# Optimization experiments

Measured on AMD Instinct MI355X. Metric: run time of the kernel, lower is better.

The kernel has to match this reference:

```python
import jax, jax.numpy as jnp
import numpy as np

B, C, D = 512, 1000, 512
K = 10


def setup_inputs() -> dict:
    key = jax.random.key(0)
    k1, k2, k3, k4, k5 = jax.random.split(key, 5)
    x = jax.random.normal(k1, (B, D), dtype=jnp.float32)
    protos = jax.random.normal(k2, (C, D), dtype=jnp.float32)
    # ex2/ex1 chosen so N*ex2^2 - ex1^2 > 0 (valid sqrt)
    ex2 = jax.random.uniform(k3, (C, D), dtype=jnp.float32) + 1.0
    ex1 = jax.random.uniform(k4, (C, D), dtype=jnp.float32) * 0.1
    cls_num = jax.random.randint(k5, (C,), 1, 100, dtype=jnp.int32)
    proto_label = jnp.arange(C, dtype=jnp.int32)
    return {"x": x, "protos": protos, "ex2": ex2, "ex1": ex1,
            "cls_num": cls_num, "proto_label": proto_label, "k_nearest": K}


def reference(x, protos, ex2, ex1, cls_num, proto_label, k_nearest):
    # rd: per-class, per-feature variance proxy  [C, D]
    N = cls_num[:, None].astype(ex2.dtype)
    rd = jnp.sqrt(N * ex2 ** 2 - ex1 ** 2)
    # softmax over feature dim of (rowmax - rd)
    rd = jax.nn.softmax(jnp.max(rd, axis=1, keepdims=True) - rd, axis=1)
    # weighted squared distances: [B, C, D] -> reduce D -> [B, C]
    diff = x[:, None, :] - protos[None, :, :]
    x_dists = diff ** 2 * rd[None, :, :]
    simi_mat = x_dists.sum(axis=2)  # [B, C]
    # k smallest distances (torch.topk largest=False)
    neg_vals, topk_index = jax.lax.top_k(-simi_mat, k_nearest)
    topk_vals = -neg_vals  # [B, K]
    topk_conf = topk_vals.sum(axis=1, keepdims=True) / topk_vals  # [B, K]
    # pick prototype with max confidence, map through label table
    temp = jnp.argmax(topk_conf, axis=1)  # [B]
    ans_index = jnp.take_along_axis(topk_index, temp[:, None], axis=1)[:, 0]
    predict = proto_label[ans_index]  # [B]
    return predict, topk_conf
```

## Files before the change

kernel.cpp:

```cpp
#include <hip/hip_runtime.h>
#include <math.h>
#include <float.h>

#define B_SZ 512
#define C_SZ 1000
#define D_SZ 512
#define K_TOP 10
#define K2 1024

#define SIMI_OFF 0

#define BM 128
#define BN 16
#define BK 64
#define LDB 1032

using f16x8 = __attribute__((ext_vector_type(8))) _Float16;
using f32x4 = __attribute__((ext_vector_type(4))) float;

#if __has_builtin(__builtin_amdgcn_exp2f)
#define FAST_EXP2(x) __builtin_amdgcn_exp2f(x)
#else
#define FAST_EXP2(x) exp2f(x)
#endif
#if __has_builtin(__builtin_amdgcn_sqrtf)
#define FAST_SQRT(x) __builtin_amdgcn_sqrtf(x)
#else
#define FAST_SQRT(x) sqrtf(x)
#endif
#define LOG2E 1.44269504088896340736f

__device__ __forceinline__ void split2(float v, _Float16& h, _Float16& l) {
    h = (_Float16)v;
    l = (_Float16)(v - (float)h);
}

__global__ __launch_bounds__(512, 4) void fused_kernel(const float* __restrict__ x,
                                                       const float* __restrict__ protos,
                                                       const float* __restrict__ ex2,
                                                       const float* __restrict__ ex1,
                                                       const int* __restrict__ cls_num,
                                                       float* __restrict__ simi) {
    __shared__ __align__(16) _Float16 BSh[BN][LDB];
    __shared__ __align__(16) _Float16 BSl[BN][LDB];
    __shared__ float t3s[BN];

    const int tid  = threadIdx.x;
    const int lane = tid & 63;
    const int w    = tid >> 6;
    const int cx = blockIdx.x & 63;
    const int by = blockIdx.x >> 6;
    const int c0 = cx * BN;
    const int b0 = by * BM;
    if (c0 >= C_SZ) return;

    const int mw = w * 16;
    const int lr = lane & 15;
    const int kg = lane >> 4;

    const float* xrow = x + (size_t)(b0 + mw + lr) * D_SZ;

    auto load_a = [&](int ch, float4* d) {
        const int kx = (ch < 8 ? ch * BK : ch * BK - D_SZ) + kg * 8;
        const float* xp = xrow + kx;
        d[0] = *(const float4*)(xp);
        d[1] = *(const float4*)(xp + 4);
        d[2] = *(const float4*)(xp + 32);
        d[3] = *(const float4*)(xp + 36);
    };

    float4 cur[4], nxt[4];
    load_a(0, cur);

    #pragma unroll
    for (int r = 0; r < 2; r++) {
        const int lc = w * 2 + r;
        const int c  = c0 + lc;
        if (c < C_SZ) {
            const size_t rb = (size_t)c * D_SZ + lane * 8;
            float e2v[8], e1v[8], pv[8];
            *(float4*)&e2v[0] = *(const float4*)(ex2 + rb);
            *(float4*)&e2v[4] = *(const float4*)(ex2 + rb + 4);
            *(float4*)&e1v[0] = *(const float4*)(ex1 + rb);
            *(float4*)&e1v[4] = *(const float4*)(ex1 + rb + 4);
            *(float4*)&pv[0]  = *(const float4*)(protos + rb);
            *(float4*)&pv[4]  = *(const float4*)(protos + rb + 4);
            const float N = (float)cls_num[c];

            float v[8], mn = FLT_MAX;
            #pragma unroll
            for (int k = 0; k < 8; k++) {
                v[k] = FAST_SQRT(N * e2v[k] * e2v[k] - e1v[k] * e1v[k]);
                mn = fminf(mn, v[k]);
            }
            #pragma unroll
            for (int off = 1; off < 64; off <<= 1) mn = fminf(mn, __shfl_xor(mn, off));

            float ev[8], s = 0.f, te = 0.f;
            #pragma unroll
            for (int k = 0; k < 8; k++) {
                ev[k] = FAST_EXP2((mn - v[k]) * LOG2E);
                s += ev[k];
                te = fmaf(ev[k] * pv[k], pv[k], te);
            }
            #pragma unroll
            for (int off = 1; off < 64; off <<= 1) {
                s  += __shfl_xor(s, off);
                te += __shfl_xor(te, off);
            }
            const float inv = 1.0f / s;
            if (lane == 0) t3s[lc] = te * inv;

            f16x8 h1, l1, h2, l2;
            #pragma unroll
            for (int k = 0; k < 8; k++) {
                const float rdv = ev[k] * inv;
                const float w2  = -2.0f * rdv * pv[k];
                _Float16 hh, ll;
                split2(rdv, hh, ll); h1[k] = hh; l1[k] = ll;
                split2(w2,  hh, ll); h2[k] = hh; l2[k] = ll;
            }
            const int d = lane * 8;
            *(f16x8*)&BSh[lc][d]         = h1;
            *(f16x8*)&BSh[lc][D_SZ + d]  = h2;
            *(f16x8*)&BSl[lc][d]         = l1;
            *(f16x8*)&BSl[lc][D_SZ + d]  = l2;
        } else {
            f16x8 z;
            #pragma unroll
            for (int k = 0; k < 8; k++) z[k] = (_Float16)0.f;
            const int d = lane * 8;
            *(f16x8*)&BSh[lc][d]        = z;
            *(f16x8*)&BSh[lc][D_SZ + d] = z;
            *(f16x8*)&BSl[lc][d]        = z;
            *(f16x8*)&BSl[lc][D_SZ + d] = z;
        }
    }
    __syncthreads();

    f32x4 acc;
    #pragma unroll
    for (int r = 0; r < 4; r++) acc[r] = 0.f;

    for (int ch = 0; ch < K2 / BK; ch++) {
        if (ch + 1 < K2 / BK) load_a(ch + 1, nxt);

        float av[16];
        *(float4*)&av[0]  = cur[0];
        *(float4*)&av[4]  = cur[1];
        *(float4*)&av[8]  = cur[2];
        *(float4*)&av[12] = cur[3];
        if (ch < 8) {
            #pragma unroll
            for (int k = 0; k < 16; k++) av[k] *= av[k];
        }
        f16x8 ah0, al0, ah1, al1;
        #pragma unroll
        for (int k = 0; k < 8; k++) {
            _Float16 hh, ll;
            split2(av[k], hh, ll);     ah0[k] = hh; al0[k] = ll;
            split2(av[k + 8], hh, ll); ah1[k] = hh; al1[k] = ll;
        }

        const int kb = ch * BK + kg * 8;
        {
            const f16x8 fbh = *(const f16x8*)&BSh[lr][kb];
            const f16x8 fbl = *(const f16x8*)&BSl[lr][kb];
            acc = __builtin_amdgcn_mfma_f32_16x16x32_f16(al0, fbl, acc, 0, 0, 0);
            acc = __builtin_amdgcn_mfma_f32_16x16x32_f16(ah0, fbl, acc, 0, 0, 0);
            acc = __builtin_amdgcn_mfma_f32_16x16x32_f16(al0, fbh, acc, 0, 0, 0);
            acc = __builtin_amdgcn_mfma_f32_16x16x32_f16(ah0, fbh, acc, 0, 0, 0);
        }
        {
            const f16x8 fbh = *(const f16x8*)&BSh[lr][kb + 32];
            const f16x8 fbl = *(const f16x8*)&BSl[lr][kb + 32];
            acc = __builtin_amdgcn_mfma_f32_16x16x32_f16(al1, fbl, acc, 0, 0, 0);
            acc = __builtin_amdgcn_mfma_f32_16x16x32_f16(ah1, fbl, acc, 0, 0, 0);
            acc = __builtin_amdgcn_mfma_f32_16x16x32_f16(al1, fbh, acc, 0, 0, 0);
            acc = __builtin_amdgcn_mfma_f32_16x16x32_f16(ah1, fbh, acc, 0, 0, 0);
        }

        if (ch + 1 < K2 / BK) {
            cur[0] = nxt[0]; cur[1] = nxt[1];
            cur[2] = nxt[2]; cur[3] = nxt[3];
        }
    }

    const int c = c0 + lr;
    if (c < C_SZ) {
        const float t3v = t3s[lr];
        #pragma unroll
        for (int r = 0; r < 4; r++) {
            const int b = b0 + mw + kg * 4 + r;
            simi[(size_t)b * C_SZ + c] = acc[r] + t3v;
        }
    }
}

__global__ __launch_bounds__(256) void topk_kernel(const float* __restrict__ ws,
                                                   const int* __restrict__ proto_label,
                                                   float* __restrict__ out) {
    const float* simi = ws + SIMI_OFF;
    const int wid = threadIdx.x >> 6;
    const int lane = threadIdx.x & 63;
    const int b = blockIdx.x * 4 + wid;

    float vals[16];
    #pragma unroll
    for (int j = 0; j < 16; j++) {
        const int c = lane + j * 64;
        vals[j] = (c < C_SZ) ? simi[(size_t)b * C_SZ + c] : FLT_MAX;
    }

    float kv[K_TOP];
    int ki[K_TOP];
    for (int t = 0; t < K_TOP; t++) {
        float bv = FLT_MAX;
        int bi = 0x7fffffff;
        #pragma unroll
        for (int j = 0; j < 16; j++) {
            const int c = lane + j * 64;
            if (vals[j] < bv) { bv = vals[j]; bi = c; }
        }
        #pragma unroll
        for (int off = 1; off < 64; off <<= 1) {
            const float ov = __shfl_xor(bv, off);
            const int oi = __shfl_xor(bi, off);
            if (ov < bv || (ov == bv && oi < bi)) { bv = ov; bi = oi; }
        }
        kv[t] = bv;
        ki[t] = bi;
        if ((bi & 63) == lane) vals[bi >> 6] = FLT_MAX;
    }

    if (lane == 0) {
        float S = 0.f;
        #pragma unroll
        for (int t = 0; t < K_TOP; t++) S += kv[t];
        float conf[K_TOP];
        #pragma unroll
        for (int t = 0; t < K_TOP; t++) {
            conf[t] = S / kv[t];
            out[B_SZ + b * K_TOP + t] = conf[t];
        }
        int best = 0;
        for (int t = 1; t < K_TOP; t++)
            if (conf[t] > conf[best]) best = t;
        out[b] = (float)proto_label[ki[best]];
    }
}

extern "C" void kernel_launch(void* const* d_in, const int* in_sizes, int n_in,
                              void* d_out, int out_size, void* d_ws, size_t ws_size,
                              hipStream_t stream) {
    const float* x           = (const float*)d_in[0];
    const float* protos      = (const float*)d_in[1];
    const float* ex2         = (const float*)d_in[2];
    const float* ex1         = (const float*)d_in[3];
    const int*   cls_num     = (const int*)d_in[4];
    const int*   proto_label = (const int*)d_in[5];

    float* ws  = (float*)d_ws;
    float* out = (float*)d_out;

    fused_kernel<<<256, 512, 0, stream>>>(x, protos, ex2, ex1, cls_num,
                                          ws + SIMI_OFF);

    topk_kernel<<<B_SZ / 4, 256, 0, stream>>>(ws, proto_label, out);
}
```

Measured before the change: 96.35 us.

## Halve class tile to 8 per block and load x once per chunk

The fused distance kernel now handles 8 classes per block instead of 16. The MFMA B tile is padded with zero rows, and the grid is a 2D 125x4 launch with no out-of-range blocks, so 500 blocks run instead of 256 and work is spread over more CUs. The main loop now loads each x chunk once and feeds both x^2 and x into the MFMAs, halving the global reads of x per block. The cost is that half of each 16-wide MFMA computes padding, and the per-block prototype preprocessing is repeated across more blocks.

```diff
diff --git a/kernel.cpp b/kernel.cpp
--- a/kernel.cpp
+++ b/kernel.cpp
@@ -11,8 +11,8 @@
 #define SIMI_OFF 0
 
 #define BM 128
-#define BN 16
-#define BK 64
+#define BN 8
+#define BNP 16
 #define LDB 1032
 
 using f16x8 = __attribute__((ext_vector_type(8))) _Float16;
@@ -41,18 +41,17 @@
                                                        const float* __restrict__ ex1,
                                                        const int* __restrict__ cls_num,
                                                        float* __restrict__ simi) {
-    __shared__ __align__(16) _Float16 BSh[BN][LDB];
-    __shared__ __align__(16) _Float16 BSl[BN][LDB];
+    __shared__ __align__(16) _Float16 BSh[BNP][LDB];
+    __shared__ __align__(16) _Float16 BSl[BNP][LDB];
     __shared__ float t3s[BN];
 
     const int tid  = threadIdx.x;
     const int lane = tid & 63;
     const int w    = tid >> 6;
-    const int cx = blockIdx.x & 63;
-    const int by = blockIdx.x >> 6;
+    const int cx = blockIdx.x;
+    const int by = blockIdx.y;
     const int c0 = cx * BN;
     const int b0 = by * BM;
-    if (c0 >= C_SZ) return;
 
     const int mw = w * 16;
     const int lr = lane & 15;
@@ -61,8 +60,7 @@
     const float* xrow = x + (size_t)(b0 + mw + lr) * D_SZ;
 
     auto load_a = [&](int ch, float4* d) {
-        const int kx = (ch < 8 ? ch * BK : ch * BK - D_SZ) + kg * 8;
-        const float* xp = xrow + kx;
+        const float* xp = xrow + ch * 64 + kg * 8;
         d[0] = *(const float4*)(xp);
         d[1] = *(const float4*)(xp + 4);
         d[2] = *(const float4*)(xp + 32);
@@ -72,69 +70,65 @@
     float4 cur[4], nxt[4];
     load_a(0, cur);
 
-    #pragma unroll
-    for (int r = 0; r < 2; r++) {
-        const int lc = w * 2 + r;
+    {
+        const int lc = w;
         const int c  = c0 + lc;
-        if (c < C_SZ) {
-            const size_t rb = (size_t)c * D_SZ + lane * 8;
-            float e2v[8], e1v[8], pv[8];
-            *(float4*)&e2v[0] = *(const float4*)(ex2 + rb);
-            *(float4*)&e2v[4] = *(const float4*)(ex2 + rb + 4);
-            *(float4*)&e1v[0] = *(const float4*)(ex1 + rb);
-            *(float4*)&e1v[4] = *(const float4*)(ex1 + rb + 4);
-            *(float4*)&pv[0]  = *(const float4*)(protos + rb);
-            *(float4*)&pv[4]  = *(const float4*)(protos + rb + 4);
-            const float N = (float)cls_num[c];
-
-            float v[8], mn = FLT_MAX;
-            #pragma unroll
-            for (int k = 0; k < 8; k++) {
-                v[k] = FAST_SQRT(N * e2v[k] * e2v[k] - e1v[k] * e1v[k]);
-                mn = fminf(mn, v[k]);
-            }
-            #pragma unroll
-            for (int off = 1; off < 64; off <<= 1) mn = fminf(mn, __shfl_xor(mn, off));
-
-            float ev[8], s = 0.f, te = 0.f;
-            #pragma unroll
-            for (int k = 0; k < 8; k++) {
-                ev[k] = FAST_EXP2((mn - v[k]) * LOG2E);
-                s += ev[k];
-                te = fmaf(ev[k] * pv[k], pv[k], te);
-            }
-            #pragma unroll
-            for (int off = 1; off < 64; off <<= 1) {
-                s  += __shfl_xor(s, off);
-                te += __shfl_xor(te, off);
-            }
-            const float inv = 1.0f / s;
-            if (lane == 0) t3s[lc] = te * inv;
-
-            f16x8 h1, l1, h2, l2;
-            #pragma unroll
-            for (int k = 0; k < 8; k++) {
-                const float rdv = ev[k] * inv;
-                const float w2  = -2.0f * rdv * pv[k];
-                _Float16 hh, ll;
-                split2(rdv, hh, ll); h1[k] = hh; l1[k] = ll;
-                split2(w2,  hh, ll); h2[k] = hh; l2[k] = ll;
-            }
-            const int d = lane * 8;
-            *(f16x8*)&BSh[lc][d]         = h1;
-            *(f16x8*)&BSh[lc][D_SZ + d]  = h2;
-            *(f16x8*)&BSl[lc][d]         = l1;
-            *(f16x8*)&BSl[lc][D_SZ + d]  = l2;
-        } else {
-            f16x8 z;
-            #pragma unroll
-            for (int k = 0; k < 8; k++) z[k] = (_Float16)0.f;
-            const int d = lane * 8;
-            *(f16x8*)&BSh[lc][d]        = z;
-            *(f16x8*)&BSh[lc][D_SZ + d] = z;
-            *(f16x8*)&BSl[lc][d]        = z;
-            *(f16x8*)&BSl[lc][D_SZ + d] = z;
-        }
+        const size_t rb = (size_t)c * D_SZ + lane * 8;
+        float e2v[8], e1v[8], pv[8];
+        *(float4*)&e2v[0] = *(const float4*)(ex2 + rb);
+        *(float4*)&e2v[4] = *(const float4*)(ex2 + rb + 4);
+        *(float4*)&e1v[0] = *(const float4*)(ex1 + rb);
+        *(float4*)&e1v[4] = *(const float4*)(ex1 + rb + 4);
+        *(float4*)&pv[0]  = *(const float4*)(protos + rb);
+        *(float4*)&pv[4]  = *(const float4*)(protos + rb + 4);
+        const float N = (float)cls_num[c];
+
+        float v[8], mn = FLT_MAX;
+        #pragma unroll
+        for (int k = 0; k < 8; k++) {
+            v[k] = FAST_SQRT(N * e2v[k] * e2v[k] - e1v[k] * e1v[k]);
+            mn = fminf(mn, v[k]);
+        }
+        #pragma unroll
+        for (int off = 1; off < 64; off <<= 1) mn = fminf(mn, __shfl_xor(mn, off));
+
+        float ev[8], s = 0.f, te = 0.f;
+        #pragma unroll
+        for (int k = 0; k < 8; k++) {
+            ev[k] = FAST_EXP2((mn - v[k]) * LOG2E);
+            s += ev[k];
+            te = fmaf(ev[k] * pv[k], pv[k], te);
+        }
+        #pragma unroll
+        for (int off = 1; off < 64; off <<= 1) {
+            s  += __shfl_xor(s, off);
+            te += __shfl_xor(te, off);
+        }
+        const float inv = 1.0f / s;
+        if (lane == 0) t3s[lc] = te * inv;
+
+        f16x8 h1, l1, h2, l2;
+        #pragma unroll
+        for (int k = 0; k < 8; k++) {
+            const float rdv = ev[k] * inv;
+            const float w2  = -2.0f * rdv * pv[k];
+            _Float16 hh, ll;
+            split2(rdv, hh, ll); h1[k] = hh; l1[k] = ll;
+            split2(w2,  hh, ll); h2[k] = hh; l2[k] = ll;
+        }
+        const int d = lane * 8;
+        *(f16x8*)&BSh[lc][d]         = h1;
+        *(f16x8*)&BSh[lc][D_SZ + d]  = h2;
+        *(f16x8*)&BSl[lc][d]         = l1;
+        *(f16x8*)&BSl[lc][D_SZ + d]  = l2;
+
+        f16x8 z;
+        #pragma unroll
+        for (int k = 0; k < 8; k++) z[k] = (_Float16)0.f;
+        *(f16x8*)&BSh[8 + lc][d]        = z;
+        *(f16x8*)&BSh[8 + lc][D_SZ + d] = z;
+        *(f16x8*)&BSl[8 + lc][d]        = z;
+        *(f16x8*)&BSl[8 + lc][D_SZ + d] = z;
     }
     __syncthreads();
 
@@ -142,52 +136,75 @@
     #pragma unroll
     for (int r = 0; r < 4; r++) acc[r] = 0.f;
 
-    for (int ch = 0; ch < K2 / BK; ch++) {
-        if (ch + 1 < K2 / BK) load_a(ch + 1, nxt);
+    for (int ch = 0; ch < 8; ch++) {
+        if (ch + 1 < 8) load_a(ch + 1, nxt);
 
         float av[16];
         *(float4*)&av[0]  = cur[0];
         *(float4*)&av[4]  = cur[1];
         *(float4*)&av[8]  = cur[2];
         *(float4*)&av[12] = cur[3];
-        if (ch < 8) {
-            #pragma unroll
-            for (int k = 0; k < 16; k++) av[k] *= av[k];
-        }
-        f16x8 ah0, al0, ah1, al1;
+
+        f16x8 rh0, rl0, rh1, rl1;
         #pragma unroll
         for (int k = 0; k < 8; k++) {
             _Float16 hh, ll;
-            split2(av[k], hh, ll);     ah0[k] = hh; al0[k] = ll;
-            split2(av[k + 8], hh, ll); ah1[k] = hh; al1[k] = ll;
-        }
-
-        const int kb = ch * BK + kg * 8;
-        {
-            const f16x8 fbh = *(const f16x8*)&BSh[lr][kb];
-            const f16x8 fbl = *(const f16x8*)&BSl[lr][kb];
-            acc = __builtin_amdgcn_mfma_f32_16x16x32_f16(al0, fbl, acc, 0, 0, 0);
-            acc = __builtin_amdgcn_mfma_f32_16x16x32_f16(ah0, fbl, acc, 0, 0, 0);
-            acc = __builtin_amdgcn_mfma_f32_16x16x32_f16(al0, fbh, acc, 0, 0, 0);
-            acc = __builtin_amdgcn_mfma_f32_16x16x32_f16(ah0, fbh, acc, 0, 0, 0);
-        }
-        {
-            const f16x8 fbh = *(const f16x8*)&BSh[lr][kb + 32];
-            const f16x8 fbl = *(const f16x8*)&BSl[lr][kb + 32];
-            acc = __builtin_amdgcn_mfma_f32_16x16x32_f16(al1, fbl, acc, 0, 0, 0);
-            acc = __builtin_amdgcn_mfma_f32_16x16x32_f16(ah1, fbl, acc, 0, 0, 0);
-            acc = __builtin_amdgcn_mfma_f32_16x16x32_f16(al1, fbh, acc, 0, 0, 0);
-            acc = __builtin_amdgcn_mfma_f32_16x16x32_f16(ah1, fbh, acc, 0, 0, 0);
-        }
-
-        if (ch + 1 < K2 / BK) {
+            split2(av[k], hh, ll);     rh0[k] = hh; rl0[k] = ll;
+            split2(av[k + 8], hh, ll); rh1[k] = hh; rl1[k] = ll;
+        }
+        f16x8 sh0, sl0, sh1, sl1;
+        #pragma unroll
+        for (int k = 0; k < 8; k++) {
+            _Float16 hh, ll;
+            const float q0 = av[k] * av[k];
+            const float q1 = av[k + 8] * av[k + 8];
+            split2(q0, hh, ll); sh0[k] = hh; sl0[k] = ll;
+            split2(q1, hh, ll); sh1[k] = hh; sl1[k] = ll;
+        }
+
+        const int kbS = ch * 64 + kg * 8;
+        const int kbR = D_SZ + kbS;
+        {
+            const f16x8 fbh = *(const f16x8*)&BSh[lr][kbS];
+            const f16x8 fbl = *(const f16x8*)&BSl[lr][kbS];
+            acc = __builtin_amdgcn_mfma_f32_16x16x32_f16(sl0, fbl, acc, 0, 0, 0);
+            acc = __builtin_amdgcn_mfma_f32_16x16x32_f16(sh0, fbl, acc, 0, 0, 0);
+            acc = __builtin_amdgcn_mfma_f32_16x16x32_f16(sl0, fbh, acc, 0, 0, 0);
+            acc = __builtin_amdgcn_mfma_f32_16x16x32_f16(sh0, fbh, acc, 0, 0, 0);
+        }
+        {
+            const f16x8 fbh = *(const f16x8*)&BSh[lr][kbS + 32];
+            const f16x8 fbl = *(const f16x8*)&BSl[lr][kbS + 32];
+            acc = __builtin_amdgcn_mfma_f32_16x16x32_f16(sl1, fbl, acc, 0, 0, 0);
+            acc = __builtin_amdgcn_mfma_f32_16x16x32_f16(sh1, fbl, acc, 0, 0, 0);
+            acc = __builtin_amdgcn_mfma_f32_16x16x32_f16(sl1, fbh, acc, 0, 0, 0);
+            acc = __builtin_amdgcn_mfma_f32_16x16x32_f16(sh1, fbh, acc, 0, 0, 0);
+        }
+        {
+            const f16x8 fbh = *(const f16x8*)&BSh[lr][kbR];
+            const f16x8 fbl = *(const f16x8*)&BSl[lr][kbR];
+            acc = __builtin_amdgcn_mfma_f32_16x16x32_f16(rl0, fbl, acc, 0, 0, 0);
+            acc = __builtin_amdgcn_mfma_f32_16x16x32_f16(rh0, fbl, acc, 0, 0, 0);
+            acc = __builtin_amdgcn_mfma_f32_16x16x32_f16(rl0, fbh, acc, 0, 0, 0);
+            acc = __builtin_amdgcn_mfma_f32_16x16x32_f16(rh0, fbh, acc, 0, 0, 0);
+        }
+        {
+            const f16x8 fbh = *(const f16x8*)&BSh[lr][kbR + 32];
+            const f16x8 fbl = *(const f16x8*)&BSl[lr][kbR + 32];
+            acc = __builtin_amdgcn_mfma_f32_16x16x32_f16(rl1, fbl, acc, 0, 0, 0);
+            acc = __builtin_amdgcn_mfma_f32_16x16x32_f16(rh1, fbl, acc, 0, 0, 0);
+            acc = __builtin_amdgcn_mfma_f32_16x16x32_f16(rl1, fbh, acc, 0, 0, 0);
+            acc = __builtin_amdgcn_mfma_f32_16x16x32_f16(rh1, fbh, acc, 0, 0, 0);
+        }
+
+        if (ch + 1 < 8) {
             cur[0] = nxt[0]; cur[1] = nxt[1];
             cur[2] = nxt[2]; cur[3] = nxt[3];
         }
     }
 
-    const int c = c0 + lr;
-    if (c < C_SZ) {
+    if (lr < BN) {
+        const int c = c0 + lr;
         const float t3v = t3s[lr];
         #pragma unroll
         for (int r = 0; r < 4; r++) {
@@ -263,8 +280,8 @@
     float* ws  = (float*)d_ws;
     float* out = (float*)d_out;
 
-    fused_kernel<<<256, 512, 0, stream>>>(x, protos, ex2, ex1, cls_num,
-                                          ws + SIMI_OFF);
+    fused_kernel<<<dim3(125, 4), 512, 0, stream>>>(x, protos, ex2, ex1, cls_num,
+                                                   ws + SIMI_OFF);
 
     topk_kernel<<<B_SZ / 4, 256, 0, stream>>>(ws, proto_label, out);
 }
```

After: 100.6 us. 4.4% more time.
